# Performance work log

Measured on AMD Instinct MI355X. Metric: run time of the kernel, lower is better.

## Reference

```python
import jax, jax.numpy as jnp
import numpy as np

N = 50000   # nodes
E = 800000  # edges (avg degree 16)
D = 64      # isize == hidden_dim
L = 3       # num_gc_layers
BN_EPS = 1e-5


def setup_inputs() -> dict:
    key = jax.random.key(0)
    ks = jax.random.split(key, 8)
    x = jax.random.normal(ks[0], (N, D), dtype=jnp.float32)
    edge_index = jax.random.randint(ks[1], (2, E), 0, N, dtype=jnp.int64)
    # Stacked per-layer MLP params (layer 0 has isize==hidden_dim so shapes match)
    scale = 0.05
    W1 = jax.random.normal(ks[2], (L, D, D), dtype=jnp.float32) * scale
    b1 = jax.random.normal(ks[3], (L, D), dtype=jnp.float32) * scale
    W2 = jax.random.normal(ks[4], (L, D, D), dtype=jnp.float32) * scale
    b2 = jax.random.normal(ks[5], (L, D), dtype=jnp.float32) * scale
    gamma = jnp.ones((L, D), dtype=jnp.float32)
    beta = jnp.zeros((L, D), dtype=jnp.float32)
    return {"x": x, "edge_index": edge_index, "W1": W1, "b1": b1,
            "W2": W2, "b2": b2, "gamma": gamma, "beta": beta}


def reference(x, edge_index, W1, b1, W2, b2, gamma, beta):
    # GINConv (eps=0): h_i' = MLP(x_i + sum_{j->i} x_j), then BatchNorm1d
    # (training-mode batch statistics), ReLU on all but the last layer.
    # Dropout is identity (deterministic / eval).
    src = edge_index[0]
    dst = edge_index[1]
    h = x
    for i in range(L):
        agg = jax.ops.segment_sum(h[src], dst, num_segments=N)  # [N, D] scatter-add
        z = h + agg                                             # (1+eps)*x + agg, eps=0
        z = jnp.maximum(z @ W1[i] + b1[i], 0.0)                 # MLP hidden + ReLU
        z = z @ W2[i] + b2[i]                                   # MLP out
        mean = jnp.mean(z, axis=0)
        var = jnp.var(z, axis=0)                                # biased var, as torch BN
        z = (z - mean) * jax.lax.rsqrt(var + BN_EPS) * gamma[i] + beta[i]
        if i < L - 1:
            z = jnp.maximum(z, 0.0)
        h = z
    return h
```

## Files before the change

### kernel.cpp

```cpp
#include <hip/hip_runtime.h>

#define NN 50000
#define EE 800000
#define DD 64
#define BN_EPS 1e-5f

#define NPART 8
#define PART_NODES 6250
#define CAP 64
#define BCAP 131072
#define NSCAT 32
#define NB_BUCKET 782
#define NB_AGG  12500
#define NB_MLP  782
#define NB_ELT8 1563
#define NB_APPLY 3125

typedef __attribute__((ext_vector_type(8))) short short8v;
typedef __attribute__((ext_vector_type(4))) float float4v;

__device__ __forceinline__ unsigned bfpack2(float a, float b) {
    union { float f; unsigned u; } ua, ub;
    ua.f = a; ub.f = b;
    unsigned ra = ua.u + 0x7fffu + ((ua.u >> 16) & 1u);
    unsigned rb = ub.u + 0x7fffu + ((ub.u >> 16) & 1u);
    return (ra >> 16) | (rb & 0xffff0000u);
}

__device__ __forceinline__ unsigned short bf16of(float v) {
    union { float f; unsigned u; } x; x.f = v;
    unsigned r = x.u + 0x7fffu + ((x.u >> 16) & 1u);
    return (unsigned short)(r >> 16);
}

__global__ void k_zero_small(int* __restrict__ bucketCnt, float* __restrict__ stats) {
    int t = threadIdx.x;
    if (t < 128) bucketCnt[t] = 0;
    if (t < 384) stats[t] = 0.f;
}

__global__ __launch_bounds__(1024) void k_build(const int* __restrict__ src,
                                                const int* __restrict__ dst,
                                                unsigned long long* __restrict__ bucket,
                                                int* __restrict__ bucketCnt,
                                                int* __restrict__ cursor) {
    __shared__ int lcnt[8];
    __shared__ int lbase[8];
    int t = threadIdx.x;
    int g = blockIdx.x * 1024 + t;
    if (g < NN) cursor[g] = 0;
    if (t < 8) lcnt[t] = 0;
    __syncthreads();
    int d = 0, s = 0, p = 0, loc = 0;
    bool ok = (g < EE);
    if (ok) {
        d = __builtin_nontemporal_load(dst + g);
        s = __builtin_nontemporal_load(src + g);
        p = (unsigned)d / PART_NODES;
        loc = atomicAdd(&lcnt[p], 1);
    }
    __syncthreads();
    if (t < 8) lbase[t] = atomicAdd(&bucketCnt[t * 16], lcnt[t]);
    __syncthreads();
    if (ok) {
        unsigned long long v = ((unsigned long long)(unsigned)s << 32) | (unsigned)d;
        bucket[(size_t)p * BCAP + lbase[p] + loc] = v;
    }
}

__global__ __launch_bounds__(256) void k_scatter(const unsigned long long* __restrict__ bucket,
                                                 const int* __restrict__ bucketCnt,
                                                 int* __restrict__ cursor,
                                                 int* __restrict__ col) {
    int p = blockIdx.x & 7;
    int cnt = bucketCnt[p * 16];
    const unsigned long long* b = bucket + (size_t)p * BCAP;
    for (int i = (blockIdx.x >> 3) * 256 + threadIdx.x; i < cnt; i += NSCAT * 256) {
        unsigned long long v = __builtin_nontemporal_load(b + i);
        int d = (int)(v & 0xffffffffu);
        int s = (int)(v >> 32);
        int pos = atomicAdd(&cursor[d], 1);
        col[d * CAP + pos] = s;
    }
}

__global__ __launch_bounds__(256) void k_cvt(const float* __restrict__ x,
                                             unsigned* __restrict__ xb) {
    int t = blockIdx.x * 256 + threadIdx.x;
    if (t >= NN * 8) return;
    const float4* p = (const float4*)(x + (size_t)t * 8);
    float4 a = p[0], b = p[1];
    uint4 o;
    o.x = bfpack2(a.x, a.y); o.y = bfpack2(a.z, a.w);
    o.z = bfpack2(b.x, b.y); o.w = bfpack2(b.z, b.w);
    ((uint4*)xb)[t] = o;
}

__global__ void k_prepw(const float* __restrict__ W1, const float* __restrict__ W2,
                        unsigned short* __restrict__ Wb) {
    int idx = blockIdx.x * 256 + threadIdx.x;
    if (idx >= 3 * 2 * 4096) return;
    int l = idx / 8192;
    int rem = idx - l * 8192;
    int m = rem / 4096;
    int e = rem - m * 4096;
    int c = e >> 6, k = e & 63;
    const float* W = (m == 0 ? W1 : W2) + l * 4096;
    Wb[idx] = bf16of(W[k * 64 + c]);
}

__global__ __launch_bounds__(256) void k_agg4(const unsigned* __restrict__ hb,
                                              const int* __restrict__ deg,
                                              const int* __restrict__ col,
                                              unsigned* __restrict__ outZb) {
    int node = blockIdx.x * 4 + (threadIdx.x >> 6);
    int lane = threadIdx.x & 63;
    int li = lane & 7;
    int slot = lane >> 3;
    int dn = deg[node];
    int base = node * CAP;
    const uint4* hb4 = (const uint4*)hb;
    float acc[8];
#pragma unroll
    for (int i = 0; i < 8; ++i) acc[i] = 0.f;

#define UNPK_ADD(U)                                                      \
    {                                                                    \
        uint4 _u = (U);                                                  \
        union { unsigned u; float f; } l0, h0, l1, h1, l2, h2, l3, h3;   \
        l0.u = _u.x << 16; h0.u = _u.x & 0xffff0000u;                    \
        l1.u = _u.y << 16; h1.u = _u.y & 0xffff0000u;                    \
        l2.u = _u.z << 16; h2.u = _u.z & 0xffff0000u;                    \
        l3.u = _u.w << 16; h3.u = _u.w & 0xffff0000u;                    \
        acc[0] += l0.f; acc[1] += h0.f; acc[2] += l1.f; acc[3] += h1.f;  \
        acc[4] += l2.f; acc[5] += h2.f; acc[6] += l3.f; acc[7] += h3.f;  \
    }

    if (slot == 0)
        UNPK_ADD(hb4[(size_t)node * 8 + li]);

    int k = slot;
    for (; k + 8 < dn; k += 16) {
        int s0 = __builtin_nontemporal_load(col + base + k);
        int s1 = __builtin_nontemporal_load(col + base + k + 8);
        uint4 u0 = hb4[(size_t)s0 * 8 + li];
        uint4 u1 = hb4[(size_t)s1 * 8 + li];
        UNPK_ADD(u0);
        UNPK_ADD(u1);
    }
    if (k < dn) {
        int s0 = __builtin_nontemporal_load(col + base + k);
        UNPK_ADD(hb4[(size_t)s0 * 8 + li]);
    }
#undef UNPK_ADD

#pragma unroll
    for (int i = 0; i < 8; ++i) acc[i] += __shfl_xor(acc[i], 8);
#pragma unroll
    for (int i = 0; i < 8; ++i) acc[i] += __shfl_xor(acc[i], 16);
#pragma unroll
    for (int i = 0; i < 8; ++i) acc[i] += __shfl_xor(acc[i], 32);

    if (slot == 0) {
        uint4 o;
        o.x = bfpack2(acc[0], acc[1]);
        o.y = bfpack2(acc[2], acc[3]);
        o.z = bfpack2(acc[4], acc[5]);
        o.w = bfpack2(acc[6], acc[7]);
        ((uint4*)outZb)[(size_t)node * 8 + li] = o;
    }
}

__global__ __launch_bounds__(256) void k_mlp_mfma(const unsigned short* __restrict__ Zb,
                                                  const unsigned short* __restrict__ WbL,
                                                  const float* __restrict__ b1,
                                                  const float* __restrict__ b2,
                                                  float* __restrict__ Zf) {
    __shared__ unsigned short sm[4][16 * 72];
    int w = threadIdx.x >> 6;
    int lane = threadIdx.x & 63;
    int q = lane >> 4;
    int cl = lane & 15;
    int r0 = blockIdx.x * 64 + w * 16;

    short8v B1[4][2], B2[4][2];
#pragma unroll
    for (int t = 0; t < 4; ++t) {
#pragma unroll
        for (int h = 0; h < 2; ++h) {
            B1[t][h] = *(const short8v*)(WbL + ((t * 16 + cl) * 64 + h * 32 + q * 8));
            B2[t][h] = *(const short8v*)(WbL + 4096 + ((t * 16 + cl) * 64 + h * 32 + q * 8));
        }
    }

    const unsigned short* zr = Zb + (size_t)(r0 + cl) * 64;
    short8v a0 = *(const short8v*)(zr + q * 8);
    short8v a1 = *(const short8v*)(zr + 32 + q * 8);

    float4v acc1[4];
#pragma unroll
    for (int t = 0; t < 4; ++t) {
        float b = b1[t * 16 + cl];
        acc1[t] = (float4v){b, b, b, b};
        acc1[t] = __builtin_amdgcn_mfma_f32_16x16x32_bf16(a0, B1[t][0], acc1[t], 0, 0, 0);
        acc1[t] = __builtin_amdgcn_mfma_f32_16x16x32_bf16(a1, B1[t][1], acc1[t], 0, 0, 0);
    }

    unsigned short* s = sm[w];
#pragma unroll
    for (int t = 0; t < 4; ++t) {
#pragma unroll
        for (int r = 0; r < 4; ++r) {
            float v = fmaxf(acc1[t][r], 0.f);
            s[(q * 4 + r) * 72 + t * 16 + cl] = bf16of(v);
        }
    }

    short8v a2_0 = *(const short8v*)(s + cl * 72 + q * 8);
    short8v a2_1 = *(const short8v*)(s + cl * 72 + 32 + q * 8);

    float4v acc2[4];
#pragma unroll
    for (int t = 0; t < 4; ++t) {
        float b = b2[t * 16 + cl];
        acc2[t] = (float4v){b, b, b, b};
        acc2[t] = __builtin_amdgcn_mfma_f32_16x16x32_bf16(a2_0, B2[t][0], acc2[t], 0, 0, 0);
        acc2[t] = __builtin_amdgcn_mfma_f32_16x16x32_bf16(a2_1, B2[t][1], acc2[t], 0, 0, 0);
    }

#pragma unroll
    for (int t = 0; t < 4; ++t) {
#pragma unroll
        for (int r = 0; r < 4; ++r) {
            int row = r0 + q * 4 + r;
            if (row < NN) Zf[(size_t)row * 64 + t * 16 + cl] = acc2[t][r];
        }
    }
}

__global__ __launch_bounds__(256) void k_stats(const float* __restrict__ B,
                                               float* __restrict__ statsL) {
    __shared__ float ssum[256];
    __shared__ float sss[256];
    int t = threadIdx.x;
    int g = blockIdx.x * 256 + t;
    int c = g & 63;
    int rs = g >> 6;
    int stride = (gridDim.x * 256) >> 6;
    float sum = 0.f, ss = 0.f;
    for (int r = rs; r < NN; r += stride) {
        float v = B[(size_t)r * 64 + c];
        sum += v;
        ss = fmaf(v, v, ss);
    }
    ssum[t] = sum;
    sss[t] = ss;
    __syncthreads();
    if (t < 64) {
        float s4 = ssum[t] + ssum[t + 64] + ssum[t + 128] + ssum[t + 192];
        float q4 = sss[t] + sss[t + 64] + sss[t + 128] + sss[t + 192];
        atomicAdd(&statsL[t], s4);
        atomicAdd(&statsL[64 + t], q4);
    }
}

__global__ __launch_bounds__(256) void k_bnapply16(const float* __restrict__ Z,
                                                   const float* __restrict__ statsL,
                                                   const float* __restrict__ gammaL,
                                                   const float* __restrict__ betaL,
                                                   unsigned* __restrict__ hb) {
    __shared__ float sa[64];
    __shared__ float sc[64];
    int tt = threadIdx.x;
    if (tt < 64) {
        float mean = statsL[tt] * (1.f / NN);
        float var = statsL[64 + tt] * (1.f / NN) - mean * mean;
        float a = gammaL[tt] * rsqrtf(var + BN_EPS);
        sa[tt] = a;
        sc[tt] = fmaf(-mean, a, betaL[tt]);
    }
    __syncthreads();
    int t = blockIdx.x * 256 + tt;
    if (t >= NN * 8) return;
    int cb = (t & 7) * 8;
    const float4* p = (const float4*)(Z + (size_t)t * 8);
    float4 a = p[0], b = p[1];
    a.x = fmaxf(fmaf(a.x, sa[cb + 0], sc[cb + 0]), 0.f);
    a.y = fmaxf(fmaf(a.y, sa[cb + 1], sc[cb + 1]), 0.f);
    a.z = fmaxf(fmaf(a.z, sa[cb + 2], sc[cb + 2]), 0.f);
    a.w = fmaxf(fmaf(a.w, sa[cb + 3], sc[cb + 3]), 0.f);
    b.x = fmaxf(fmaf(b.x, sa[cb + 4], sc[cb + 4]), 0.f);
    b.y = fmaxf(fmaf(b.y, sa[cb + 5], sc[cb + 5]), 0.f);
    b.z = fmaxf(fmaf(b.z, sa[cb + 6], sc[cb + 6]), 0.f);
    b.w = fmaxf(fmaf(b.w, sa[cb + 7], sc[cb + 7]), 0.f);
    uint4 o;
    o.x = bfpack2(a.x, a.y); o.y = bfpack2(a.z, a.w);
    o.z = bfpack2(b.x, b.y); o.w = bfpack2(b.z, b.w);
    ((uint4*)hb)[t] = o;
}

__global__ __launch_bounds__(256) void k_apply_aff(const float* __restrict__ B,
                                                   const float* __restrict__ statsL,
                                                   const float* __restrict__ gammaL,
                                                   const float* __restrict__ betaL,
                                                   float* __restrict__ out) {
    __shared__ float sa[64];
    __shared__ float sc[64];
    int t = threadIdx.x;
    if (t < 64) {
        float mean = statsL[t] * (1.f / NN);
        float var = statsL[64 + t] * (1.f / NN) - mean * mean;
        float a = gammaL[t] * rsqrtf(var + BN_EPS);
        sa[t] = a;
        sc[t] = fmaf(-mean, a, betaL[t]);
    }
    __syncthreads();
    int i4 = blockIdx.x * 256 + t;
    if (i4 >= NN * 16) return;
    int cb = (i4 & 15) * 4;
    float4 v = ((const float4*)B)[i4];
    float4 o;
    o.x = fmaf(v.x, sa[cb + 0], sc[cb + 0]);
    o.y = fmaf(v.y, sa[cb + 1], sc[cb + 1]);
    o.z = fmaf(v.z, sa[cb + 2], sc[cb + 2]);
    o.w = fmaf(v.w, sa[cb + 3], sc[cb + 3]);
    ((float4*)out)[i4] = o;
}

extern "C" void kernel_launch(void* const* d_in, const int* in_sizes, int n_in,
                              void* d_out, int out_size, void* d_ws, size_t ws_size,
                              hipStream_t stream) {
    const float* x     = (const float*)d_in[0];
    const int*   ei    = (const int*)d_in[1];
    const float* W1    = (const float*)d_in[2];
    const float* b1    = (const float*)d_in[3];
    const float* W2    = (const float*)d_in[4];
    const float* b2    = (const float*)d_in[5];
    const float* gamma = (const float*)d_in[6];
    const float* beta  = (const float*)d_in[7];
    float* out = (float*)d_out;

    const int* src = ei;
    const int* dst = ei + EE;

    char* w = (char*)d_ws;
    unsigned*       Zb  = (unsigned*)w;       w += (size_t)(NN + 64) * DD * 2;
    float*          Zf  = (float*)w;          w += (size_t)NN * DD * 4;
    unsigned*       Hb  = (unsigned*)w;       w += (size_t)NN * DD * 2;
    unsigned*       Xb  = (unsigned*)w;       w += (size_t)NN * DD * 2;
    int*            col = (int*)w;            w += (size_t)NN * CAP * 4;
    unsigned long long* bucket = (unsigned long long*)w;
    w += (size_t)NPART * BCAP * 8;
    int*            cursor    = (int*)w;      w += (size_t)NN * 4;
    int*            bucketCnt = (int*)w;      w += 128 * 4;
    float*          stats     = (float*)w;    w += 384 * 4;
    unsigned short* Wb        = (unsigned short*)w; w += 3 * 2 * 4096 * 2;

    k_zero_small<<<1, 512, 0, stream>>>(bucketCnt, stats);
    k_build<<<NB_BUCKET, 1024, 0, stream>>>(src, dst, bucket, bucketCnt, cursor);
    k_cvt<<<NB_ELT8, 256, 0, stream>>>(x, Xb);
    k_prepw<<<96, 256, 0, stream>>>(W1, W2, Wb);
    k_scatter<<<NPART * NSCAT, 256, 0, stream>>>(bucket, bucketCnt, cursor, col);

    k_agg4<<<NB_AGG, 256, 0, stream>>>(Xb, cursor, col, Zb);
    k_mlp_mfma<<<NB_MLP, 256, 0, stream>>>((unsigned short*)Zb, Wb, b1, b2, Zf);
    k_stats<<<256, 256, 0, stream>>>(Zf, stats);
    k_bnapply16<<<NB_ELT8, 256, 0, stream>>>(Zf, stats, gamma, beta, Hb);

    k_agg4<<<NB_AGG, 256, 0, stream>>>(Hb, cursor, col, Zb);
    k_mlp_mfma<<<NB_MLP, 256, 0, stream>>>((unsigned short*)Zb, Wb + 8192, b1 + 64, b2 + 64, Zf);
    k_stats<<<256, 256, 0, stream>>>(Zf, stats + 128);
    k_bnapply16<<<NB_ELT8, 256, 0, stream>>>(Zf, stats + 128, gamma + 64, beta + 64, Hb);

    k_agg4<<<NB_AGG, 256, 0, stream>>>(Hb, cursor, col, Zb);
    k_mlp_mfma<<<NB_MLP, 256, 0, stream>>>((unsigned short*)Zb, Wb + 16384, b1 + 128, b2 + 128, Zf);
    k_stats<<<256, 256, 0, stream>>>(Zf, stats + 256);
    k_apply_aff<<<NB_APPLY, 256, 0, stream>>>(Zf, stats + 256, gamma + 128, beta + 128, out);
}
```

Before: 245.2 us.

## Split bf16 features into column halves, fuse BN stats into MLP, merge setup kernels

The bf16 node features are stored as two column-half arrays (32 columns each), and aggregation runs twice per layer, once per half. The goal is a gather working set per pass that fits better in cache (about 3.2MB instead of 6.4MB), improving hit rates for random neighbor gathers. BatchNorm sum and sum-of-squares are now reduced inside the MLP kernel with shuffles, shared memory and atomics, which removes the separate stats pass over Zf. The x/W conversion and zeroing kernels are merged into one setup kernel. The trade-off is twice as many passes over the col index array and extra kernel launches for aggregation.

```diff
diff --git a/kernel.cpp b/kernel.cpp
--- a/kernel.cpp
+++ b/kernel.cpp
@@ -1,6 +1,7 @@
 #include <hip/hip_runtime.h>
 
 #define NN 50000
+#define NPAD 50064
 #define EE 800000
 #define DD 64
 #define BN_EPS 1e-5f
@@ -13,6 +14,7 @@
 #define NB_BUCKET 782
 #define NB_AGG  12500
 #define NB_MLP  782
+#define NB_SETUP 1563
 #define NB_ELT8 1563
 #define NB_APPLY 3125
 
@@ -33,10 +35,36 @@
     return (unsigned short)(r >> 16);
 }
 
-__global__ void k_zero_small(int* __restrict__ bucketCnt, float* __restrict__ stats) {
-    int t = threadIdx.x;
+__global__ __launch_bounds__(256) void k_setup(const float* __restrict__ x,
+                                               unsigned* __restrict__ xb0,
+                                               unsigned* __restrict__ xb1,
+                                               const float* __restrict__ W1,
+                                               const float* __restrict__ W2,
+                                               unsigned short* __restrict__ Wb,
+                                               int* __restrict__ bucketCnt,
+                                               float* __restrict__ stats) {
+    int t = blockIdx.x * 256 + threadIdx.x;
+    if (t < NN * 8) {
+        int row = t >> 3, c8 = t & 7;
+        const float4* p = (const float4*)(x + (size_t)row * 64 + c8 * 8);
+        float4 a = p[0], b = p[1];
+        uint4 o;
+        o.x = bfpack2(a.x, a.y); o.y = bfpack2(a.z, a.w);
+        o.z = bfpack2(b.x, b.y); o.w = bfpack2(b.z, b.w);
+        unsigned* dp = (c8 < 4) ? xb0 : xb1;
+        ((uint4*)dp)[(size_t)row * 4 + (c8 & 3)] = o;
+    }
+    if (t < 3 * 2 * 4096) {
+        int l = t / 8192;
+        int rem = t - l * 8192;
+        int m = rem / 4096;
+        int e = rem - m * 4096;
+        int c = e >> 6, k = e & 63;
+        const float* W = (m == 0 ? W1 : W2) + l * 4096;
+        Wb[t] = bf16of(W[k * 64 + c]);
+    }
     if (t < 128) bucketCnt[t] = 0;
-    if (t < 384) stats[t] = 0.f;
+    else if (t < 512) stats[t - 128] = 0.f;
 }
 
 __global__ __launch_bounds__(1024) void k_build(const int* __restrict__ src,
@@ -84,42 +112,17 @@
     }
 }
 
-__global__ __launch_bounds__(256) void k_cvt(const float* __restrict__ x,
-                                             unsigned* __restrict__ xb) {
-    int t = blockIdx.x * 256 + threadIdx.x;
-    if (t >= NN * 8) return;
-    const float4* p = (const float4*)(x + (size_t)t * 8);
-    float4 a = p[0], b = p[1];
-    uint4 o;
-    o.x = bfpack2(a.x, a.y); o.y = bfpack2(a.z, a.w);
-    o.z = bfpack2(b.x, b.y); o.w = bfpack2(b.z, b.w);
-    ((uint4*)xb)[t] = o;
-}
-
-__global__ void k_prepw(const float* __restrict__ W1, const float* __restrict__ W2,
-                        unsigned short* __restrict__ Wb) {
-    int idx = blockIdx.x * 256 + threadIdx.x;
-    if (idx >= 3 * 2 * 4096) return;
-    int l = idx / 8192;
-    int rem = idx - l * 8192;
-    int m = rem / 4096;
-    int e = rem - m * 4096;
-    int c = e >> 6, k = e & 63;
-    const float* W = (m == 0 ? W1 : W2) + l * 4096;
-    Wb[idx] = bf16of(W[k * 64 + c]);
-}
-
-__global__ __launch_bounds__(256) void k_agg4(const unsigned* __restrict__ hb,
+__global__ __launch_bounds__(256) void k_agg5(const unsigned* __restrict__ hbH,
                                               const int* __restrict__ deg,
                                               const int* __restrict__ col,
-                                              unsigned* __restrict__ outZb) {
+                                              unsigned* __restrict__ outH) {
     int node = blockIdx.x * 4 + (threadIdx.x >> 6);
     int lane = threadIdx.x & 63;
-    int li = lane & 7;
-    int slot = lane >> 3;
+    int li = lane & 3;
+    int slot = lane >> 2;
     int dn = deg[node];
     int base = node * CAP;
-    const uint4* hb4 = (const uint4*)hb;
+    const uint4* hb4 = (const uint4*)hbH;
     float acc[8];
 #pragma unroll
     for (int i = 0; i < 8; ++i) acc[i] = 0.f;
@@ -137,24 +140,17 @@
     }
 
     if (slot == 0)
-        UNPK_ADD(hb4[(size_t)node * 8 + li]);
-
-    int k = slot;
-    for (; k + 8 < dn; k += 16) {
-        int s0 = __builtin_nontemporal_load(col + base + k);
-        int s1 = __builtin_nontemporal_load(col + base + k + 8);
-        uint4 u0 = hb4[(size_t)s0 * 8 + li];
-        uint4 u1 = hb4[(size_t)s1 * 8 + li];
-        UNPK_ADD(u0);
-        UNPK_ADD(u1);
-    }
-    if (k < dn) {
-        int s0 = __builtin_nontemporal_load(col + base + k);
-        UNPK_ADD(hb4[(size_t)s0 * 8 + li]);
+        UNPK_ADD(hb4[(size_t)node * 4 + li]);
+
+    for (int k = slot; k < dn; k += 16) {
+        int s = __builtin_nontemporal_load(col + base + k);
+        UNPK_ADD(hb4[(size_t)s * 4 + li]);
     }
 #undef UNPK_ADD
 
 #pragma unroll
+    for (int i = 0; i < 8; ++i) acc[i] += __shfl_xor(acc[i], 4);
+#pragma unroll
     for (int i = 0; i < 8; ++i) acc[i] += __shfl_xor(acc[i], 8);
 #pragma unroll
     for (int i = 0; i < 8; ++i) acc[i] += __shfl_xor(acc[i], 16);
@@ -162,21 +158,26 @@
     for (int i = 0; i < 8; ++i) acc[i] += __shfl_xor(acc[i], 32);
 
     if (slot == 0) {
-        uint4 o;
-        o.x = bfpack2(acc[0], acc[1]);
-        o.y = bfpack2(acc[2], acc[3]);
-        o.z = bfpack2(acc[4], acc[5]);
-        o.w = bfpack2(acc[6], acc[7]);
-        ((uint4*)outZb)[(size_t)node * 8 + li] = o;
-    }
-}
-
-__global__ __launch_bounds__(256) void k_mlp_mfma(const unsigned short* __restrict__ Zb,
+        unsigned p0 = bfpack2(acc[0], acc[1]);
+        unsigned p1 = bfpack2(acc[2], acc[3]);
+        unsigned p2 = bfpack2(acc[4], acc[5]);
+        unsigned p3 = bfpack2(acc[6], acc[7]);
+        unsigned long long* q =
+            (unsigned long long*)(outH + ((size_t)node * 4 + li) * 4);
+        __builtin_nontemporal_store(((unsigned long long)p1 << 32) | p0, q);
+        __builtin_nontemporal_store(((unsigned long long)p3 << 32) | p2, q + 1);
+    }
+}
+
+__global__ __launch_bounds__(256) void k_mlp_mfma(const unsigned short* __restrict__ Zb0,
+                                                  const unsigned short* __restrict__ Zb1,
                                                   const unsigned short* __restrict__ WbL,
                                                   const float* __restrict__ b1,
                                                   const float* __restrict__ b2,
-                                                  float* __restrict__ Zf) {
+                                                  float* __restrict__ Zf,
+                                                  float* __restrict__ statsL) {
     __shared__ unsigned short sm[4][16 * 72];
+    __shared__ float sred[2][4][64];
     int w = threadIdx.x >> 6;
     int lane = threadIdx.x & 63;
     int q = lane >> 4;
@@ -193,9 +194,9 @@
         }
     }
 
-    const unsigned short* zr = Zb + (size_t)(r0 + cl) * 64;
-    short8v a0 = *(const short8v*)(zr + q * 8);
-    short8v a1 = *(const short8v*)(zr + 32 + q * 8);
+    int arow = r0 + cl;
+    short8v a0 = *(const short8v*)(Zb0 + (size_t)arow * 32 + q * 8);
+    short8v a1 = *(const short8v*)(Zb1 + (size_t)arow * 32 + q * 8);
 
     float4v acc1[4];
 #pragma unroll
@@ -236,31 +237,31 @@
             if (row < NN) Zf[(size_t)row * 64 + t * 16 + cl] = acc2[t][r];
         }
     }
-}
-
-__global__ __launch_bounds__(256) void k_stats(const float* __restrict__ B,
-                                               float* __restrict__ statsL) {
-    __shared__ float ssum[256];
-    __shared__ float sss[256];
-    int t = threadIdx.x;
-    int g = blockIdx.x * 256 + t;
-    int c = g & 63;
-    int rs = g >> 6;
-    int stride = (gridDim.x * 256) >> 6;
-    float sum = 0.f, ss = 0.f;
-    for (int r = rs; r < NN; r += stride) {
-        float v = B[(size_t)r * 64 + c];
-        sum += v;
-        ss = fmaf(v, v, ss);
-    }
-    ssum[t] = sum;
-    sss[t] = ss;
-    __syncthreads();
-    if (t < 64) {
-        float s4 = ssum[t] + ssum[t + 64] + ssum[t + 128] + ssum[t + 192];
-        float q4 = sss[t] + sss[t + 64] + sss[t + 128] + sss[t + 192];
-        atomicAdd(&statsL[t], s4);
-        atomicAdd(&statsL[64 + t], q4);
+
+#pragma unroll
+    for (int t = 0; t < 4; ++t) {
+        float sv = 0.f, qv = 0.f;
+#pragma unroll
+        for (int r = 0; r < 4; ++r) {
+            int row = r0 + q * 4 + r;
+            float v = (row < NN) ? acc2[t][r] : 0.f;
+            sv += v;
+            qv = fmaf(v, v, qv);
+        }
+        sv += __shfl_xor(sv, 16); sv += __shfl_xor(sv, 32);
+        qv += __shfl_xor(qv, 16); qv += __shfl_xor(qv, 32);
+        if (lane < 16) {
+            sred[0][w][t * 16 + cl] = sv;
+            sred[1][w][t * 16 + cl] = qv;
+        }
+    }
+    __syncthreads();
+    int tt = threadIdx.x;
+    if (tt < 128) {
+        int which = tt >> 6, c = tt & 63;
+        float tot = sred[which][0][c] + sred[which][1][c] +
+                    sred[which][2][c] + sred[which][3][c];
+        atomicAdd(&statsL[which * 64 + c], tot);
     }
 }
 
@@ -268,7 +269,8 @@
                                                    const float* __restrict__ statsL,
                                                    const float* __restrict__ gammaL,
                                                    const float* __restrict__ betaL,
-                                                   unsigned* __restrict__ hb) {
+                                                   unsigned* __restrict__ hb0,
+                                                   unsigned* __restrict__ hb1) {
     __shared__ float sa[64];
     __shared__ float sc[64];
     int tt = threadIdx.x;
@@ -282,8 +284,9 @@
     __syncthreads();
     int t = blockIdx.x * 256 + tt;
     if (t >= NN * 8) return;
-    int cb = (t & 7) * 8;
-    const float4* p = (const float4*)(Z + (size_t)t * 8);
+    int row = t >> 3, c8 = t & 7;
+    int cb = c8 * 8;
+    const float4* p = (const float4*)(Z + (size_t)row * 64 + cb);
     float4 a = p[0], b = p[1];
     a.x = fmaxf(fmaf(a.x, sa[cb + 0], sc[cb + 0]), 0.f);
     a.y = fmaxf(fmaf(a.y, sa[cb + 1], sc[cb + 1]), 0.f);
@@ -296,7 +299,8 @@
     uint4 o;
     o.x = bfpack2(a.x, a.y); o.y = bfpack2(a.z, a.w);
     o.z = bfpack2(b.x, b.y); o.w = bfpack2(b.z, b.w);
-    ((uint4*)hb)[t] = o;
+    unsigned* dp = (c8 < 4) ? hb0 : hb1;
+    ((uint4*)dp)[(size_t)row * 4 + (c8 & 3)] = o;
 }
 
 __global__ __launch_bounds__(256) void k_apply_aff(const float* __restrict__ B,
@@ -344,36 +348,40 @@
     const int* dst = ei + EE;
 
     char* w = (char*)d_ws;
-    unsigned*       Zb  = (unsigned*)w;       w += (size_t)(NN + 64) * DD * 2;
-    float*          Zf  = (float*)w;          w += (size_t)NN * DD * 4;
-    unsigned*       Hb  = (unsigned*)w;       w += (size_t)NN * DD * 2;
-    unsigned*       Xb  = (unsigned*)w;       w += (size_t)NN * DD * 2;
-    int*            col = (int*)w;            w += (size_t)NN * CAP * 4;
+    unsigned* Zb0 = (unsigned*)w; w += (size_t)NPAD * 32 * 2;
+    unsigned* Zb1 = (unsigned*)w; w += (size_t)NPAD * 32 * 2;
+    unsigned* Hb0 = (unsigned*)w; w += (size_t)NPAD * 32 * 2;
+    unsigned* Hb1 = (unsigned*)w; w += (size_t)NPAD * 32 * 2;
+    unsigned* Xb0 = (unsigned*)w; w += (size_t)NPAD * 32 * 2;
+    unsigned* Xb1 = (unsigned*)w; w += (size_t)NPAD * 32 * 2;
+    float*    Zf  = (float*)w;    w += (size_t)NN * DD * 4;
+    int*      col = (int*)w;      w += (size_t)NN * CAP * 4;
     unsigned long long* bucket = (unsigned long long*)w;
     w += (size_t)NPART * BCAP * 8;
-    int*            cursor    = (int*)w;      w += (size_t)NN * 4;
-    int*            bucketCnt = (int*)w;      w += 128 * 4;
-    float*          stats     = (float*)w;    w += 384 * 4;
-    unsigned short* Wb        = (unsigned short*)w; w += 3 * 2 * 4096 * 2;
-
-    k_zero_small<<<1, 512, 0, stream>>>(bucketCnt, stats);
+    int*      cursor    = (int*)w; w += (size_t)NN * 4;
+    int*      bucketCnt = (int*)w; w += 128 * 4;
+    float*    stats     = (float*)w; w += 384 * 4;
+    unsigned short* Wb  = (unsigned short*)w; w += 3 * 2 * 4096 * 2;
+
+    k_setup<<<NB_SETUP, 256, 0, stream>>>(x, Xb0, Xb1, W1, W2, Wb, bucketCnt, stats);
     k_build<<<NB_BUCKET, 1024, 0, stream>>>(src, dst, bucket, bucketCnt, cursor);
-    k_cvt<<<NB_ELT8, 256, 0, stream>>>(x, Xb);
-    k_prepw<<<96, 256, 0, stream>>>(W1, W2, Wb);
     k_scatter<<<NPART * NSCAT, 256, 0, stream>>>(bucket, bucketCnt, cursor, col);
 
-    k_agg4<<<NB_AGG, 256, 0, stream>>>(Xb, cursor, col, Zb);
-    k_mlp_mfma<<<NB_MLP, 256, 0, stream>>>((unsigned short*)Zb, Wb, b1, b2, Zf);
-    k_stats<<<256, 256, 0, stream>>>(Zf, stats);
-    k_bnapply16<<<NB_ELT8, 256, 0, stream>>>(Zf, stats, gamma, beta, Hb);
-
-    k_agg4<<<NB_AGG, 256, 0, stream>>>(Hb, cursor, col, Zb);
-    k_mlp_mfma<<<NB_MLP, 256, 0, stream>>>((unsigned short*)Zb, Wb + 8192, b1 + 64, b2 + 64, Zf);
-    k_stats<<<256, 256, 0, stream>>>(Zf, stats + 128);
-    k_bnapply16<<<NB_ELT8, 256, 0, stream>>>(Zf, stats + 128, gamma + 64, beta + 64, Hb);
-
-    k_agg4<<<NB_AGG, 256, 0, stream>>>(Hb, cursor, col, Zb);
-    k_mlp_mfma<<<NB_MLP, 256, 0, stream>>>((unsigned short*)Zb, Wb + 16384, b1 + 128, b2 + 128, Zf);
-    k_stats<<<256, 256, 0, stream>>>(Zf, stats + 256);
+    k_agg5<<<NB_AGG, 256, 0, stream>>>(Xb0, cursor, col, Zb0);
+    k_agg5<<<NB_AGG, 256, 0, stream>>>(Xb1, cursor, col, Zb1);
+    k_mlp_mfma<<<NB_MLP, 256, 0, stream>>>((unsigned short*)Zb0, (unsigned short*)Zb1,
+                                           Wb, b1, b2, Zf, stats);
+    k_bnapply16<<<NB_ELT8, 256, 0, stream>>>(Zf, stats, gamma, beta, Hb0, Hb1);
+
+    k_agg5<<<NB_AGG, 256, 0, stream>>>(Hb0, cursor, col, Zb0);
+    k_agg5<<<NB_AGG, 256, 0, stream>>>(Hb1, cursor, col, Zb1);
+    k_mlp_mfma<<<NB_MLP, 256, 0, stream>>>((unsigned short*)Zb0, (unsigned short*)Zb1,
+                                           Wb + 8192, b1 + 64, b2 + 64, Zf, stats + 128);
+    k_bnapply16<<<NB_ELT8, 256, 0, stream>>>(Zf, stats + 128, gamma + 64, beta + 64, Hb0, Hb1);
+
+    k_agg5<<<NB_AGG, 256, 0, stream>>>(Hb0, cursor, col, Zb0);
+    k_agg5<<<NB_AGG, 256, 0, stream>>>(Hb1, cursor, col, Zb1);
+    k_mlp_mfma<<<NB_MLP, 256, 0, stream>>>((unsigned short*)Zb0, (unsigned short*)Zb1,
+                                           Wb + 16384, b1 + 128, b2 + 128, Zf, stats + 256);
     k_apply_aff<<<NB_APPLY, 256, 0, stream>>>(Zf, stats + 256, gamma + 128, beta + 128, out);
 }
```

After: 293.6 us. 1.2x slower.
